# Kernel tuning notes

Measured on AMD Instinct MI355X. Metric: run time of the kernel, lower is better.

Reference implementation:

```python
import jax, jax.numpy as jnp
import numpy as np

B, T, C, H = 4, 2048, 1024, 128  # batch, block_size, n_embds, head_size


def setup_inputs() -> dict:
    key = jax.random.key(0)
    k1, k2, k3, k4 = jax.random.split(key, 4)
    x = jax.random.normal(k1, (B, T, C), dtype=jnp.float32)
    # Linear(n_embds, head_size, bias=False) weights, stored as [C, H] so q = x @ Wq
    s = C ** -0.5
    Wq = jax.random.normal(k2, (C, H), dtype=jnp.float32) * s
    Wk = jax.random.normal(k3, (C, H), dtype=jnp.float32) * s
    Wv = jax.random.normal(k4, (C, H), dtype=jnp.float32) * s
    return {"x": x, "Wq": Wq, "Wk": Wk, "Wv": Wv}


def reference(x, Wq, Wk, Wv):
    # q, k, v projections (no bias)
    q = x @ Wq  # [B, T, H]
    k = x @ Wk  # [B, T, H]
    v = x @ Wv  # [B, T, H]
    scale = q.shape[-1] ** -0.5
    wei = jnp.einsum('btd,bsd->bts', q, k) * scale  # [B, T, T]
    # causal mask: positions where tril == 0 (upper triangle) get -inf
    t = wei.shape[1]
    causal = jnp.tril(jnp.ones((t, t), dtype=bool))
    wei = jnp.where(causal, wei, -jnp.inf)
    # NOTE: source uses F.softmax(wei, dim=1) -> normalize over the QUERY axis
    wei = jax.nn.softmax(wei, axis=1)
    out = wei @ v  # [B, T, H]
    return out
```

## Files before the change

### kernel.cpp

```cpp
#include <hip/hip_runtime.h>
#include <hip/hip_bf16.h>
#include <math.h>

#define B_ 4
#define T_ 2048
#define C_ 1024
#define H_ 128
#define RCHUNK 128
#define NCHUNK (T_ / RCHUNK)
#define NSCH 32

typedef unsigned short u16;
typedef unsigned int   u32;
typedef short short8  __attribute__((ext_vector_type(8)));
typedef short short4v __attribute__((ext_vector_type(4)));
typedef float floatx4 __attribute__((ext_vector_type(4)));

__device__ __forceinline__ u16 f2bf(float f) {
    __hip_bfloat16 h = __float2bfloat16(f);
    union { __hip_bfloat16 h; u16 u; } v; v.h = h; return v.u;
}
__device__ __forceinline__ float bf2f(u16 h) {
    union { u32 u; float f; } v; v.u = ((u32)h) << 16;
    return v.f;
}

__global__ __launch_bounds__(256) void convert_w_kernel(
    const float* __restrict__ Wq, const float* __restrict__ Wk,
    const float* __restrict__ Wv, u16* __restrict__ Wt)
{
    const int k0 = blockIdx.x * 64, n0 = blockIdx.y * 64, widx = blockIdx.z;
    const float* W = (widx == 0) ? Wq : (widx == 1) ? Wk : Wv;

    __shared__ float ts[64][68];
    for (int i = threadIdx.x; i < 64 * 16; i += 256) {
        int r = i >> 4, c4 = i & 15;
        float4 v = *(const float4*)&W[(size_t)(k0 + r) * H_ + n0 + c4 * 4];
        ts[r][c4 * 4 + 0] = v.x; ts[r][c4 * 4 + 1] = v.y;
        ts[r][c4 * 4 + 2] = v.z; ts[r][c4 * 4 + 3] = v.w;
    }
    __syncthreads();
    for (int i = threadIdx.x; i < 64 * 16; i += 256) {
        int n = i >> 4, k4 = i & 15;
        short4v o;
        #pragma unroll
        for (int j = 0; j < 4; ++j) o[j] = (short)f2bf(ts[k4 * 4 + j][n]);
        *(short4v*)&Wt[(size_t)widx * H_ * C_ + (size_t)(n0 + n) * C_ + k0 + k4 * 4] = o;
    }
}

__global__ __launch_bounds__(256) void qkv_gemm_kernel(
    const float* __restrict__ x, const u16* __restrict__ Wt,
    u16* __restrict__ Qb, u16* __restrict__ Kb, u16* __restrict__ Vt)
{
    const int m0   = blockIdx.x * 64;
    const int widx = blockIdx.y;
    const u16* Wg = Wt + (size_t)widx * H_ * C_;

    __shared__ u16 As[64 * 136];
    __shared__ u16 Bs[128 * 136];

    const int w    = threadIdx.x >> 6;
    const int lane = threadIdx.x & 63;
    const int q    = lane >> 4, r = lane & 15;

    floatx4 acc[8] = {};

    for (int k0 = 0; k0 < C_; k0 += 128) {
        for (int i = threadIdx.x; i < 64 * 16; i += 256) {
            int rr = i >> 4, c = i & 15;
            const float* xg = &x[(size_t)(m0 + rr) * C_ + k0 + c * 8];
            float4 a = *(const float4*)xg;
            float4 b = *(const float4*)(xg + 4);
            short8 o;
            o[0]=(short)f2bf(a.x); o[1]=(short)f2bf(a.y);
            o[2]=(short)f2bf(a.z); o[3]=(short)f2bf(a.w);
            o[4]=(short)f2bf(b.x); o[5]=(short)f2bf(b.y);
            o[6]=(short)f2bf(b.z); o[7]=(short)f2bf(b.w);
            *(short8*)&As[rr * 136 + c * 8] = o;
        }
        for (int i = threadIdx.x; i < 128 * 16; i += 256) {
            int rr = i >> 4, c = i & 15;
            *(float4*)&Bs[rr * 136 + c * 8] =
                *(const float4*)&Wg[(size_t)rr * C_ + k0 + c * 8];
        }
        __syncthreads();

        #pragma unroll
        for (int kk = 0; kk < 4; ++kk) {
            short8 af = *(const short8*)&As[(16 * w + r) * 136 + kk * 32 + q * 8];
            #pragma unroll
            for (int nt = 0; nt < 8; ++nt) {
                short8 bf = *(const short8*)&Bs[(16 * nt + r) * 136 + kk * 32 + q * 8];
                acc[nt] = __builtin_amdgcn_mfma_f32_16x16x32_bf16(af, bf, acc[nt], 0, 0, 0);
            }
        }
        __syncthreads();
    }

    if (widx == 2) {
        const int bb  = m0 / T_;
        const int tt0 = (m0 - bb * T_) + 16 * w + q * 4;
        #pragma unroll
        for (int nt = 0; nt < 8; ++nt) {
            short4v o;
            #pragma unroll
            for (int reg = 0; reg < 4; ++reg) o[reg] = (short)f2bf(acc[nt][reg]);
            *(short4v*)&Vt[((size_t)bb * H_ + 16 * nt + r) * T_ + tt0] = o;
        }
    } else {
        u16* dst = (widx == 0) ? Qb : Kb;
        #pragma unroll
        for (int nt = 0; nt < 8; ++nt)
            #pragma unroll
            for (int reg = 0; reg < 4; ++reg) {
                int mm = m0 + 16 * w + q * 4 + reg;
                int nn = 16 * nt + r;
                dst[(size_t)mm * H_ + nn] = f2bf(acc[nt][reg]);
            }
    }
}

__global__ __launch_bounds__(256) void scores_kernel(
    const u16* __restrict__ Qb, const u16* __restrict__ Kb,
    u16* __restrict__ S, float* __restrict__ pm, float* __restrict__ pl)
{
    const int si = blockIdx.x;
    const int ti = blockIdx.y;
    const int b  = blockIdx.z;
    if (si > ti) return;
    const int t0 = ti * 128, s0 = si * 128;
    const bool diag = (si == ti);

    __shared__ u16 smem[2 * 128 * 136];
    u16* Qs = smem;
    u16* Ks = smem + 128 * 136;

    const u16* Qg = Qb + ((size_t)b * T_ + t0) * H_;
    const u16* Kg = Kb + ((size_t)b * T_ + s0) * H_;

    for (int i = threadIdx.x; i < 128 * 16; i += 256) {
        int rr = i >> 4, c = i & 15;
        *(float4*)&Qs[rr * 136 + c * 8] = *(const float4*)&Qg[(size_t)rr * H_ + c * 8];
        *(float4*)&Ks[rr * 136 + c * 8] = *(const float4*)&Kg[(size_t)rr * H_ + c * 8];
    }
    __syncthreads();

    const int w    = threadIdx.x >> 6;
    const int lane = threadIdx.x & 63;
    const int q    = lane >> 4, r = lane & 15;

    floatx4 acc[2][8] = {};
    #pragma unroll
    for (int kk = 0; kk < 4; ++kk) {
        short8 a0 = *(const short8*)&Qs[(32 * w +      r) * 136 + kk * 32 + q * 8];
        short8 a1 = *(const short8*)&Qs[(32 * w + 16 + r) * 136 + kk * 32 + q * 8];
        #pragma unroll
        for (int nt = 0; nt < 8; ++nt) {
            short8 bf = *(const short8*)&Ks[(16 * nt + r) * 136 + kk * 32 + q * 8];
            acc[0][nt] = __builtin_amdgcn_mfma_f32_16x16x32_bf16(a0, bf, acc[0][nt], 0, 0, 0);
            acc[1][nt] = __builtin_amdgcn_mfma_f32_16x16x32_bf16(a1, bf, acc[1][nt], 0, 0, 0);
        }
    }
    __syncthreads();

    u16*   tile = smem;
    float* redm = (float*)(smem + 128 * 136);
    float* redl = redm + 16 * 128;
    float* Mrow = redl + 16 * 128;

    const float scale = 0.08838834764831845f;

    #pragma unroll
    for (int nt = 0; nt < 8; ++nt) {
        const int sl = 16 * nt + r;
        float mx = -INFINITY;
        #pragma unroll
        for (int mt = 0; mt < 2; ++mt)
            #pragma unroll
            for (int reg = 0; reg < 4; ++reg) {
                const int tl = 32 * w + 16 * mt + q * 4 + reg;
                const bool vl = (!diag) || (tl >= sl);
                mx = fmaxf(mx, vl ? acc[mt][nt][reg] : -INFINITY);
            }
        redm[(4 * w + q) * 128 + sl] = mx;
    }
    __syncthreads();

    if (threadIdx.x < 128) {
        const int c = threadIdx.x;
        float M = -INFINITY;
        #pragma unroll
        for (int g = 0; g < 16; ++g) M = fmaxf(M, redm[g * 128 + c]);
        M *= scale;
        Mrow[c] = M;
        pm[((size_t)b * NCHUNK + ti) * T_ + s0 + c] = M;
    }
    __syncthreads();

    #pragma unroll
    for (int nt = 0; nt < 8; ++nt) {
        const int sl = 16 * nt + r;
        const float M = Mrow[sl];
        float sm = 0.f;
        #pragma unroll
        for (int mt = 0; mt < 2; ++mt)
            #pragma unroll
            for (int reg = 0; reg < 4; ++reg) {
                const int tl = 32 * w + 16 * mt + q * 4 + reg;
                const bool vl = (!diag) || (tl >= sl);
                const float e = vl ? __expf(acc[mt][nt][reg] * scale - M) : 0.f;
                sm += e;
                tile[tl * 136 + sl] = f2bf(e);
            }
        redl[(4 * w + q) * 128 + sl] = sm;
    }
    __syncthreads();

    if (threadIdx.x < 128) {
        const int c = threadIdx.x;
        float L = 0.f;
        #pragma unroll
        for (int g = 0; g < 16; ++g) L += redl[g * 128 + c];
        pl[((size_t)b * NCHUNK + ti) * T_ + s0 + c] = L;
    }

    for (int i = threadIdx.x; i < 128 * 16; i += 256) {
        int tl = i >> 4, cc = (i >> 3) & 1, c8 = i & 7;
        u16* Sg = S + (((size_t)b * NSCH + 2 * si + cc) * T_ + t0 + tl) * 64;
        *(float4*)&Sg[c8 * 8] = *(float4*)&tile[tl * 136 + cc * 64 + c8 * 8];
    }
}

__global__ __launch_bounds__(256) void stats_f_kernel(
    const float* __restrict__ pm, const float* __restrict__ pl,
    float* __restrict__ F)
{
    const int idx = blockIdx.x * 256 + threadIdx.x;
    const int b = idx >> 11, s = idx & (T_ - 1);
    const int c0 = s >> 7;
    const float* pmB = pm + (size_t)b * NCHUNK * T_;
    const float* plB = pl + (size_t)b * NCHUNK * T_;

    float M = -INFINITY;
    for (int c = c0; c < NCHUNK; ++c)
        M = fmaxf(M, pmB[(size_t)c * T_ + s]);
    float L = 0.f;
    for (int c = c0; c < NCHUNK; ++c) {
        const float lg = plB[(size_t)c * T_ + s];
        if (lg > 0.f) L += lg * __expf(pmB[(size_t)c * T_ + s] - M);
    }
    const float Li = 1.0f / L;

    float* FB = F + (size_t)b * NCHUNK * T_;
    #pragma unroll
    for (int c = 0; c < NCHUNK; ++c)
        FB[(size_t)c * T_ + s] = (c >= c0) ? __expf(pmB[(size_t)c * T_ + s] - M) * Li : 0.f;
}

#define RST 132
__global__ __launch_bounds__(512) void out_kernel(
    const u16* __restrict__ S, const u16* __restrict__ Vt,
    const float* __restrict__ F, float* __restrict__ out)
{
    const int b   = blockIdx.y;
    const int i   = blockIdx.x;
    const int t0A = i * 16;
    const int t0B = (127 - i) * 16;
    const int ncA = (t0A + 79) >> 6;
    const int ncB = (t0B + 79) >> 6;
    const int nct = ncA + ncB;

    const int w    = threadIdx.x >> 6;
    const int lane = threadIdx.x & 63;
    const int q    = lane >> 4, r = lane & 15;
    const int tA   = t0A + r, tB = t0B + r;

    const u16* SB  = S  + (size_t)b * NSCH * T_ * 64;
    const u16* VtB = Vt + (size_t)b * H_ * T_;

    __shared__ float fsA[T_], fsB[T_];
    __shared__ float red[8][16 * RST];

    floatx4 accA[8] = {}, accB[8] = {};
    short8 sc[2];

    int kcur = w;
    {
        const bool A = kcur < ncA;
        const int ci = A ? kcur : kcur - ncA;
        const u16* Sc = SB + ((size_t)ci * T_ + (A ? tA : tB)) * 64;
        sc[0] = *(const short8*)&Sc[q * 8];
        sc[1] = *(const short8*)&Sc[32 + q * 8];
    }

    const int tiA = t0A >> 7, tiB = t0B >> 7;
    const float* FA = F + ((size_t)b * NCHUNK + tiA) * T_;
    const float* FBg = F + ((size_t)b * NCHUNK + tiB) * T_;
    for (int idx = threadIdx.x * 4; idx < 64 * ncA; idx += 2048)
        *(float4*)&fsA[idx] = *(const float4*)&FA[idx];
    for (int idx = threadIdx.x * 4; idx < 64 * ncB; idx += 2048)
        *(float4*)&fsB[idx] = *(const float4*)&FBg[idx];
    __syncthreads();

    auto body = [&](floatx4 (&acc)[8], const float* fsrow, int s0) {
        #pragma unroll
        for (int kk = 0; kk < 2; ++kk) {
            const int sb = s0 + kk * 32 + q * 8;
            float fv[8];
            *(float4*)&fv[0] = *(const float4*)&fsrow[sb];
            *(float4*)&fv[4] = *(const float4*)&fsrow[sb + 4];
            short8 af;
            #pragma unroll
            for (int j = 0; j < 8; ++j)
                af[j] = (short)f2bf(bf2f((u16)sc[kk][j]) * fv[j]);
            #pragma unroll
            for (int nt = 0; nt < 8; ++nt) {
                short8 bf = *(const short8*)&VtB[(size_t)(16 * nt + r) * T_ + sb];
                acc[nt] = __builtin_amdgcn_mfma_f32_16x16x32_bf16(af, bf, acc[nt], 0, 0, 0);
            }
        }
    };

    while (kcur < nct) {
        const int knx = kcur + 8;
        short8 sn[2];
        if (knx < nct) {
            const bool A = knx < ncA;
            const int ci = A ? knx : knx - ncA;
            const u16* Sc = SB + ((size_t)ci * T_ + (A ? tA : tB)) * 64;
            sn[0] = *(const short8*)&Sc[q * 8];
            sn[1] = *(const short8*)&Sc[32 + q * 8];
        }

        if (kcur < ncA) body(accA, fsA, kcur * 64);
        else            body(accB, fsB, (kcur - ncA) * 64);

        sc[0] = sn[0];
        sc[1] = sn[1];
        kcur = knx;
    }

    #pragma unroll
    for (int nt = 0; nt < 8; ++nt)
        #pragma unroll
        for (int reg = 0; reg < 4; ++reg)
            red[w][(q * 4 + reg) * RST + 16 * nt + r] = accA[nt][reg];
    __syncthreads();

    float* outA = out + ((size_t)b * T_ + t0A) * H_;
    for (int idx = threadIdx.x; idx < 16 * 128; idx += 512) {
        const int row = idx >> 7, col = idx & 127;
        float sum = 0.f;
        #pragma unroll
        for (int g = 0; g < 8; ++g) sum += red[g][row * RST + col];
        outA[idx] = sum;
    }
    __syncthreads();

    #pragma unroll
    for (int nt = 0; nt < 8; ++nt)
        #pragma unroll
        for (int reg = 0; reg < 4; ++reg)
            red[w][(q * 4 + reg) * RST + 16 * nt + r] = accB[nt][reg];
    __syncthreads();

    float* outB = out + ((size_t)b * T_ + t0B) * H_;
    for (int idx = threadIdx.x; idx < 16 * 128; idx += 512) {
        const int row = idx >> 7, col = idx & 127;
        float sum = 0.f;
        #pragma unroll
        for (int g = 0; g < 8; ++g) sum += red[g][row * RST + col];
        outB[idx] = sum;
    }
}

extern "C" void kernel_launch(void* const* d_in, const int* in_sizes, int n_in,
                              void* d_out, int out_size, void* d_ws, size_t ws_size,
                              hipStream_t stream) {
    const float* x  = (const float*)d_in[0];
    const float* Wq = (const float*)d_in[1];
    const float* Wk = (const float*)d_in[2];
    const float* Wv = (const float*)d_in[3];
    float* out = (float*)d_out;

    u16*   Sb   = (u16*)d_ws;
    u16*   Wt   = Sb + (size_t)B_ * T_ * T_;
    u16*   Qb   = Wt + (size_t)3 * H_ * C_;
    u16*   Kb   = Qb + (size_t)B_ * T_ * H_;
    u16*   Vt   = Kb + (size_t)B_ * T_ * H_;
    float* F    = (float*)(Vt + (size_t)B_ * T_ * H_);

    float* pm = (float*)d_out;
    float* pl = pm + (size_t)B_ * NCHUNK * T_;

    convert_w_kernel <<<dim3(C_ / 64, H_ / 64, 3), dim3(256), 0, stream>>>(Wq, Wk, Wv, Wt);
    qkv_gemm_kernel  <<<dim3(B_ * T_ / 64, 3),     dim3(256), 0, stream>>>(x, Wt, Qb, Kb, Vt);
    scores_kernel    <<<dim3(16, 16, B_),          dim3(256), 0, stream>>>(Qb, Kb, Sb, pm, pl);
    stats_f_kernel   <<<dim3(B_ * T_ / 256),       dim3(256), 0, stream>>>(pm, pl, F);
    out_kernel       <<<dim3(64, B_),              dim3(512), 0, stream>>>(Sb, Vt, F, out);
}
```

Before: 161.7 us.

## Fuse scores, stats and output kernels into one cooperative persistent kernel

Merges the scores, stats and output kernels into a single cooperative kernel launched with 256 blocks of 512 threads. Grid-wide syncs separate the three phases, and the scores phase loops over a triangular job list. pm and pl move from the output buffer into workspace. This removes two kernel launches and their gaps, but it adds grid-sync cost, leaves most threads idle in the stats phase (only 32 threads per block), and caps scores-phase parallelism at 256 blocks.

```diff
diff --git a/kernel.cpp b/kernel.cpp
--- a/kernel.cpp
+++ b/kernel.cpp
@@ -1,6 +1,9 @@
 #include <hip/hip_runtime.h>
 #include <hip/hip_bf16.h>
+#include <hip/hip_cooperative_groups.h>
 #include <math.h>
+
+namespace cg = cooperative_groups;
 
 #define B_ 4
 #define T_ 2048
@@ -9,6 +12,8 @@
 #define RCHUNK 128
 #define NCHUNK (T_ / RCHUNK)
 #define NSCH 32
+#define NTILE 136
+#define NJOBS (B_ * NTILE)
 
 typedef unsigned short u16;
 typedef unsigned int   u32;
@@ -121,257 +126,251 @@
     }
 }
 
-__global__ __launch_bounds__(256) void scores_kernel(
+#define RST 132
+__global__ __launch_bounds__(512, 2) void fused_b_kernel(
     const u16* __restrict__ Qb, const u16* __restrict__ Kb,
-    u16* __restrict__ S, float* __restrict__ pm, float* __restrict__ pl)
+    const u16* __restrict__ Vt, u16* __restrict__ S,
+    float* __restrict__ pm, float* __restrict__ pl,
+    float* __restrict__ F, float* __restrict__ out)
 {
-    const int si = blockIdx.x;
-    const int ti = blockIdx.y;
-    const int b  = blockIdx.z;
-    if (si > ti) return;
-    const int t0 = ti * 128, s0 = si * 128;
-    const bool diag = (si == ti);
-
-    __shared__ u16 smem[2 * 128 * 136];
-    u16* Qs = smem;
-    u16* Ks = smem + 128 * 136;
-
-    const u16* Qg = Qb + ((size_t)b * T_ + t0) * H_;
-    const u16* Kg = Kb + ((size_t)b * T_ + s0) * H_;
-
-    for (int i = threadIdx.x; i < 128 * 16; i += 256) {
-        int rr = i >> 4, c = i & 15;
-        *(float4*)&Qs[rr * 136 + c * 8] = *(const float4*)&Qg[(size_t)rr * H_ + c * 8];
-        *(float4*)&Ks[rr * 136 + c * 8] = *(const float4*)&Kg[(size_t)rr * H_ + c * 8];
-    }
-    __syncthreads();
-
-    const int w    = threadIdx.x >> 6;
-    const int lane = threadIdx.x & 63;
+    __shared__ __align__(16) char smem_raw[83968];
+    cg::grid_group grid = cg::this_grid();
+
+    const int blk  = blockIdx.x;
+    const int tid  = threadIdx.x;
+    const int w    = tid >> 6;
+    const int lane = tid & 63;
     const int q    = lane >> 4, r = lane & 15;
-
-    floatx4 acc[2][8] = {};
-    #pragma unroll
-    for (int kk = 0; kk < 4; ++kk) {
-        short8 a0 = *(const short8*)&Qs[(32 * w +      r) * 136 + kk * 32 + q * 8];
-        short8 a1 = *(const short8*)&Qs[(32 * w + 16 + r) * 136 + kk * 32 + q * 8];
-        #pragma unroll
-        for (int nt = 0; nt < 8; ++nt) {
-            short8 bf = *(const short8*)&Ks[(16 * nt + r) * 136 + kk * 32 + q * 8];
-            acc[0][nt] = __builtin_amdgcn_mfma_f32_16x16x32_bf16(a0, bf, acc[0][nt], 0, 0, 0);
-            acc[1][nt] = __builtin_amdgcn_mfma_f32_16x16x32_bf16(a1, bf, acc[1][nt], 0, 0, 0);
-        }
-    }
-    __syncthreads();
-
-    u16*   tile = smem;
-    float* redm = (float*)(smem + 128 * 136);
-    float* redl = redm + 16 * 128;
-    float* Mrow = redl + 16 * 128;
-
     const float scale = 0.08838834764831845f;
 
-    #pragma unroll
-    for (int nt = 0; nt < 8; ++nt) {
-        const int sl = 16 * nt + r;
-        float mx = -INFINITY;
-        #pragma unroll
-        for (int mt = 0; mt < 2; ++mt)
-            #pragma unroll
-            for (int reg = 0; reg < 4; ++reg) {
-                const int tl = 32 * w + 16 * mt + q * 4 + reg;
-                const bool vl = (!diag) || (tl >= sl);
-                mx = fmaxf(mx, vl ? acc[mt][nt][reg] : -INFINITY);
-            }
-        redm[(4 * w + q) * 128 + sl] = mx;
-    }
-    __syncthreads();
-
-    if (threadIdx.x < 128) {
-        const int c = threadIdx.x;
+    {
+        u16* Qs = (u16*)smem_raw;
+        u16* Ks = Qs + 128 * 136;
+
+        for (int job = blk; job < NJOBS; job += 256) {
+            const int b   = job / NTILE;
+            const int rem = job - b * NTILE;
+            int ti = 0;
+            while ((ti + 1) * (ti + 2) / 2 <= rem) ++ti;
+            const int si = rem - ti * (ti + 1) / 2;
+            const int t0 = ti * 128, s0 = si * 128;
+            const bool diag = (si == ti);
+
+            const u16* Qg = Qb + ((size_t)b * T_ + t0) * H_;
+            const u16* Kg = Kb + ((size_t)b * T_ + s0) * H_;
+            for (int i = tid; i < 128 * 16; i += 512) {
+                int rr = i >> 4, c = i & 15;
+                *(float4*)&Qs[rr * 136 + c * 8] = *(const float4*)&Qg[(size_t)rr * H_ + c * 8];
+                *(float4*)&Ks[rr * 136 + c * 8] = *(const float4*)&Kg[(size_t)rr * H_ + c * 8];
+            }
+            __syncthreads();
+
+            floatx4 acc[8] = {};
+            #pragma unroll
+            for (int kk = 0; kk < 4; ++kk) {
+                short8 af = *(const short8*)&Qs[(16 * w + r) * 136 + kk * 32 + q * 8];
+                #pragma unroll
+                for (int nt = 0; nt < 8; ++nt) {
+                    short8 bf = *(const short8*)&Ks[(16 * nt + r) * 136 + kk * 32 + q * 8];
+                    acc[nt] = __builtin_amdgcn_mfma_f32_16x16x32_bf16(af, bf, acc[nt], 0, 0, 0);
+                }
+            }
+            __syncthreads();
+
+            u16*   tile = (u16*)smem_raw;
+            float* redm = (float*)(smem_raw + 34816);
+            float* redl = redm + 32 * 128;
+            float* Mrow = redl + 32 * 128;
+
+            #pragma unroll
+            for (int nt = 0; nt < 8; ++nt) {
+                const int sl = 16 * nt + r;
+                float mx = -INFINITY;
+                #pragma unroll
+                for (int reg = 0; reg < 4; ++reg) {
+                    const int tl = 16 * w + q * 4 + reg;
+                    const bool vl = (!diag) || (tl >= sl);
+                    mx = fmaxf(mx, vl ? acc[nt][reg] : -INFINITY);
+                }
+                redm[(w * 4 + q) * 128 + sl] = mx;
+            }
+            __syncthreads();
+
+            if (tid < 128) {
+                float M = -INFINITY;
+                #pragma unroll
+                for (int g = 0; g < 32; ++g) M = fmaxf(M, redm[g * 128 + tid]);
+                M *= scale;
+                Mrow[tid] = M;
+                pm[((size_t)b * NCHUNK + ti) * T_ + s0 + tid] = M;
+            }
+            __syncthreads();
+
+            #pragma unroll
+            for (int nt = 0; nt < 8; ++nt) {
+                const int sl = 16 * nt + r;
+                const float M = Mrow[sl];
+                float sm = 0.f;
+                #pragma unroll
+                for (int reg = 0; reg < 4; ++reg) {
+                    const int tl = 16 * w + q * 4 + reg;
+                    const bool vl = (!diag) || (tl >= sl);
+                    const float e = vl ? __expf(acc[nt][reg] * scale - M) : 0.f;
+                    sm += e;
+                    tile[tl * 136 + sl] = f2bf(e);
+                }
+                redl[(w * 4 + q) * 128 + sl] = sm;
+            }
+            __syncthreads();
+
+            if (tid < 128) {
+                float L = 0.f;
+                #pragma unroll
+                for (int g = 0; g < 32; ++g) L += redl[g * 128 + tid];
+                pl[((size_t)b * NCHUNK + ti) * T_ + s0 + tid] = L;
+            }
+
+            for (int i = tid; i < 128 * 16; i += 512) {
+                int tl = i >> 4, cc = (i >> 3) & 1, c8 = i & 7;
+                u16* Sg = S + (((size_t)b * NSCH + 2 * si + cc) * T_ + t0 + tl) * 64;
+                *(float4*)&Sg[c8 * 8] = *(float4*)&tile[tl * 136 + cc * 64 + c8 * 8];
+            }
+            __syncthreads();
+        }
+    }
+    grid.sync();
+
+    if (tid < 32) {
+        const int p = blk * 32 + tid;
+        const int b = p >> 11, s = p & (T_ - 1);
+        const int c0 = s >> 7;
+        const float* pmB = pm + (size_t)b * NCHUNK * T_;
+        const float* plB = pl + (size_t)b * NCHUNK * T_;
         float M = -INFINITY;
-        #pragma unroll
-        for (int g = 0; g < 16; ++g) M = fmaxf(M, redm[g * 128 + c]);
-        M *= scale;
-        Mrow[c] = M;
-        pm[((size_t)b * NCHUNK + ti) * T_ + s0 + c] = M;
-    }
-    __syncthreads();
-
-    #pragma unroll
-    for (int nt = 0; nt < 8; ++nt) {
-        const int sl = 16 * nt + r;
-        const float M = Mrow[sl];
-        float sm = 0.f;
-        #pragma unroll
-        for (int mt = 0; mt < 2; ++mt)
-            #pragma unroll
-            for (int reg = 0; reg < 4; ++reg) {
-                const int tl = 32 * w + 16 * mt + q * 4 + reg;
-                const bool vl = (!diag) || (tl >= sl);
-                const float e = vl ? __expf(acc[mt][nt][reg] * scale - M) : 0.f;
-                sm += e;
-                tile[tl * 136 + sl] = f2bf(e);
-            }
-        redl[(4 * w + q) * 128 + sl] = sm;
-    }
-    __syncthreads();
-
-    if (threadIdx.x < 128) {
-        const int c = threadIdx.x;
+        for (int c = c0; c < NCHUNK; ++c)
+            M = fmaxf(M, pmB[(size_t)c * T_ + s]);
         float L = 0.f;
-        #pragma unroll
-        for (int g = 0; g < 16; ++g) L += redl[g * 128 + c];
-        pl[((size_t)b * NCHUNK + ti) * T_ + s0 + c] = L;
-    }
-
-    for (int i = threadIdx.x; i < 128 * 16; i += 256) {
-        int tl = i >> 4, cc = (i >> 3) & 1, c8 = i & 7;
-        u16* Sg = S + (((size_t)b * NSCH + 2 * si + cc) * T_ + t0 + tl) * 64;
-        *(float4*)&Sg[c8 * 8] = *(float4*)&tile[tl * 136 + cc * 64 + c8 * 8];
-    }
-}
-
-__global__ __launch_bounds__(256) void stats_f_kernel(
-    const float* __restrict__ pm, const float* __restrict__ pl,
-    float* __restrict__ F)
-{
-    const int idx = blockIdx.x * 256 + threadIdx.x;
-    const int b = idx >> 11, s = idx & (T_ - 1);
-    const int c0 = s >> 7;
-    const float* pmB = pm + (size_t)b * NCHUNK * T_;
-    const float* plB = pl + (size_t)b * NCHUNK * T_;
-
-    float M = -INFINITY;
-    for (int c = c0; c < NCHUNK; ++c)
-        M = fmaxf(M, pmB[(size_t)c * T_ + s]);
-    float L = 0.f;
-    for (int c = c0; c < NCHUNK; ++c) {
-        const float lg = plB[(size_t)c * T_ + s];
-        if (lg > 0.f) L += lg * __expf(pmB[(size_t)c * T_ + s] - M);
-    }
-    const float Li = 1.0f / L;
-
-    float* FB = F + (size_t)b * NCHUNK * T_;
-    #pragma unroll
-    for (int c = 0; c < NCHUNK; ++c)
-        FB[(size_t)c * T_ + s] = (c >= c0) ? __expf(pmB[(size_t)c * T_ + s] - M) * Li : 0.f;
-}
-
-#define RST 132
-__global__ __launch_bounds__(512) void out_kernel(
-    const u16* __restrict__ S, const u16* __restrict__ Vt,
-    const float* __restrict__ F, float* __restrict__ out)
-{
-    const int b   = blockIdx.y;
-    const int i   = blockIdx.x;
-    const int t0A = i * 16;
-    const int t0B = (127 - i) * 16;
-    const int ncA = (t0A + 79) >> 6;
-    const int ncB = (t0B + 79) >> 6;
-    const int nct = ncA + ncB;
-
-    const int w    = threadIdx.x >> 6;
-    const int lane = threadIdx.x & 63;
-    const int q    = lane >> 4, r = lane & 15;
-    const int tA   = t0A + r, tB = t0B + r;
-
-    const u16* SB  = S  + (size_t)b * NSCH * T_ * 64;
-    const u16* VtB = Vt + (size_t)b * H_ * T_;
-
-    __shared__ float fsA[T_], fsB[T_];
-    __shared__ float red[8][16 * RST];
-
-    floatx4 accA[8] = {}, accB[8] = {};
-    short8 sc[2];
-
-    int kcur = w;
+        for (int c = c0; c < NCHUNK; ++c) {
+            const float lg = plB[(size_t)c * T_ + s];
+            if (lg > 0.f) L += lg * __expf(pmB[(size_t)c * T_ + s] - M);
+        }
+        const float Li = 1.0f / L;
+        float* FB = F + (size_t)b * NCHUNK * T_;
+        #pragma unroll
+        for (int c = 0; c < NCHUNK; ++c)
+            FB[(size_t)c * T_ + s] = (c >= c0) ? __expf(pmB[(size_t)c * T_ + s] - M) * Li : 0.f;
+    }
+    grid.sync();
+
     {
-        const bool A = kcur < ncA;
-        const int ci = A ? kcur : kcur - ncA;
-        const u16* Sc = SB + ((size_t)ci * T_ + (A ? tA : tB)) * 64;
-        sc[0] = *(const short8*)&Sc[q * 8];
-        sc[1] = *(const short8*)&Sc[32 + q * 8];
-    }
-
-    const int tiA = t0A >> 7, tiB = t0B >> 7;
-    const float* FA = F + ((size_t)b * NCHUNK + tiA) * T_;
-    const float* FBg = F + ((size_t)b * NCHUNK + tiB) * T_;
-    for (int idx = threadIdx.x * 4; idx < 64 * ncA; idx += 2048)
-        *(float4*)&fsA[idx] = *(const float4*)&FA[idx];
-    for (int idx = threadIdx.x * 4; idx < 64 * ncB; idx += 2048)
-        *(float4*)&fsB[idx] = *(const float4*)&FBg[idx];
-    __syncthreads();
-
-    auto body = [&](floatx4 (&acc)[8], const float* fsrow, int s0) {
-        #pragma unroll
-        for (int kk = 0; kk < 2; ++kk) {
-            const int sb = s0 + kk * 32 + q * 8;
-            float fv[8];
-            *(float4*)&fv[0] = *(const float4*)&fsrow[sb];
-            *(float4*)&fv[4] = *(const float4*)&fsrow[sb + 4];
-            short8 af;
-            #pragma unroll
-            for (int j = 0; j < 8; ++j)
-                af[j] = (short)f2bf(bf2f((u16)sc[kk][j]) * fv[j]);
-            #pragma unroll
-            for (int nt = 0; nt < 8; ++nt) {
-                short8 bf = *(const short8*)&VtB[(size_t)(16 * nt + r) * T_ + sb];
-                acc[nt] = __builtin_amdgcn_mfma_f32_16x16x32_bf16(af, bf, acc[nt], 0, 0, 0);
-            }
-        }
-    };
-
-    while (kcur < nct) {
-        const int knx = kcur + 8;
-        short8 sn[2];
-        if (knx < nct) {
-            const bool A = knx < ncA;
-            const int ci = A ? knx : knx - ncA;
+        const int b   = blk >> 6;
+        const int i   = blk & 63;
+        const int t0A = i * 16;
+        const int t0B = (127 - i) * 16;
+        const int ncA = (t0A + 79) >> 6;
+        const int ncB = (t0B + 79) >> 6;
+        const int nct = ncA + ncB;
+
+        const int tA = t0A + r, tB = t0B + r;
+
+        const u16* SB  = S  + (size_t)b * NSCH * T_ * 64;
+        const u16* VtB = Vt + (size_t)b * H_ * T_;
+
+        float* fsA = (float*)smem_raw;
+        float* fsB = fsA + T_;
+        float* red = fsB + T_;
+
+        floatx4 accA[8] = {}, accB[8] = {};
+        short8 sc[2];
+
+        int kcur = w;
+        {
+            const bool A = kcur < ncA;
+            const int ci = A ? kcur : kcur - ncA;
             const u16* Sc = SB + ((size_t)ci * T_ + (A ? tA : tB)) * 64;
-            sn[0] = *(const short8*)&Sc[q * 8];
-            sn[1] = *(const short8*)&Sc[32 + q * 8];
-        }
-
-        if (kcur < ncA) body(accA, fsA, kcur * 64);
-        else            body(accB, fsB, (kcur - ncA) * 64);
-
-        sc[0] = sn[0];
-        sc[1] = sn[1];
-        kcur = knx;
-    }
-
-    #pragma unroll
-    for (int nt = 0; nt < 8; ++nt)
-        #pragma unroll
-        for (int reg = 0; reg < 4; ++reg)
-            red[w][(q * 4 + reg) * RST + 16 * nt + r] = accA[nt][reg];
-    __syncthreads();
-
-    float* outA = out + ((size_t)b * T_ + t0A) * H_;
-    for (int idx = threadIdx.x; idx < 16 * 128; idx += 512) {
-        const int row = idx >> 7, col = idx & 127;
-        float sum = 0.f;
-        #pragma unroll
-        for (int g = 0; g < 8; ++g) sum += red[g][row * RST + col];
-        outA[idx] = sum;
-    }
-    __syncthreads();
-
-    #pragma unroll
-    for (int nt = 0; nt < 8; ++nt)
-        #pragma unroll
-        for (int reg = 0; reg < 4; ++reg)
-            red[w][(q * 4 + reg) * RST + 16 * nt + r] = accB[nt][reg];
-    __syncthreads();
-
-    float* outB = out + ((size_t)b * T_ + t0B) * H_;
-    for (int idx = threadIdx.x; idx < 16 * 128; idx += 512) {
-        const int row = idx >> 7, col = idx & 127;
-        float sum = 0.f;
-        #pragma unroll
-        for (int g = 0; g < 8; ++g) sum += red[g][row * RST + col];
-        outB[idx] = sum;
+            sc[0] = *(const short8*)&Sc[q * 8];
+            sc[1] = *(const short8*)&Sc[32 + q * 8];
+        }
+
+        const int tiA = t0A >> 7, tiB = t0B >> 7;
+        const float* FA  = F + ((size_t)b * NCHUNK + tiA) * T_;
+        const float* FBg = F + ((size_t)b * NCHUNK + tiB) * T_;
+        for (int idx = tid * 4; idx < 64 * ncA; idx += 2048)
+            *(float4*)&fsA[idx] = *(const float4*)&FA[idx];
+        for (int idx = tid * 4; idx < 64 * ncB; idx += 2048)
+            *(float4*)&fsB[idx] = *(const float4*)&FBg[idx];
+        __syncthreads();
+
+        auto body = [&](floatx4 (&acc)[8], const float* fsrow, int s0) {
+            #pragma unroll
+            for (int kk = 0; kk < 2; ++kk) {
+                const int sb = s0 + kk * 32 + q * 8;
+                float fv[8];
+                *(float4*)&fv[0] = *(const float4*)&fsrow[sb];
+                *(float4*)&fv[4] = *(const float4*)&fsrow[sb + 4];
+                short8 af;
+                #pragma unroll
+                for (int j = 0; j < 8; ++j)
+                    af[j] = (short)f2bf(bf2f((u16)sc[kk][j]) * fv[j]);
+                #pragma unroll
+                for (int nt = 0; nt < 8; ++nt) {
+                    short8 bf = *(const short8*)&VtB[(size_t)(16 * nt + r) * T_ + sb];
+                    acc[nt] = __builtin_amdgcn_mfma_f32_16x16x32_bf16(af, bf, acc[nt], 0, 0, 0);
+                }
+            }
+        };
+
+        while (kcur < nct) {
+            const int knx = kcur + 8;
+            short8 sn[2];
+            if (knx < nct) {
+                const bool A = knx < ncA;
+                const int ci = A ? knx : knx - ncA;
+                const u16* Sc = SB + ((size_t)ci * T_ + (A ? tA : tB)) * 64;
+                sn[0] = *(const short8*)&Sc[q * 8];
+                sn[1] = *(const short8*)&Sc[32 + q * 8];
+            }
+
+            if (kcur < ncA) body(accA, fsA, kcur * 64);
+            else            body(accB, fsB, (kcur - ncA) * 64);
+
+            sc[0] = sn[0];
+            sc[1] = sn[1];
+            kcur = knx;
+        }
+
+        #pragma unroll
+        for (int nt = 0; nt < 8; ++nt)
+            #pragma unroll
+            for (int reg = 0; reg < 4; ++reg)
+                red[w * 16 * RST + (q * 4 + reg) * RST + 16 * nt + r] = accA[nt][reg];
+        __syncthreads();
+
+        float* outA = out + ((size_t)b * T_ + t0A) * H_;
+        for (int idx = tid; idx < 16 * 128; idx += 512) {
+            const int row = idx >> 7, col = idx & 127;
+            float sum = 0.f;
+            #pragma unroll
+            for (int g = 0; g < 8; ++g) sum += red[g * 16 * RST + row * RST + col];
+            outA[idx] = sum;
+        }
+        __syncthreads();
+
+        #pragma unroll
+        for (int nt = 0; nt < 8; ++nt)
+            #pragma unroll
+            for (int reg = 0; reg < 4; ++reg)
+                red[w * 16 * RST + (q * 4 + reg) * RST + 16 * nt + r] = accB[nt][reg];
+        __syncthreads();
+
+        float* outB = out + ((size_t)b * T_ + t0B) * H_;
+        for (int idx = tid; idx < 16 * 128; idx += 512) {
+            const int row = idx >> 7, col = idx & 127;
+            float sum = 0.f;
+            #pragma unroll
+            for (int g = 0; g < 8; ++g) sum += red[g * 16 * RST + row * RST + col];
+            outB[idx] = sum;
+        }
     }
 }
 
@@ -389,14 +388,15 @@
     u16*   Qb   = Wt + (size_t)3 * H_ * C_;
     u16*   Kb   = Qb + (size_t)B_ * T_ * H_;
     u16*   Vt   = Kb + (size_t)B_ * T_ * H_;
-    float* F    = (float*)(Vt + (size_t)B_ * T_ * H_);
-
-    float* pm = (float*)d_out;
-    float* pl = pm + (size_t)B_ * NCHUNK * T_;
+    float* pm   = (float*)(Vt + (size_t)B_ * T_ * H_);
+    float* pl   = pm + (size_t)B_ * NCHUNK * T_;
+    float* F    = pl + (size_t)B_ * NCHUNK * T_;
 
     convert_w_kernel <<<dim3(C_ / 64, H_ / 64, 3), dim3(256), 0, stream>>>(Wq, Wk, Wv, Wt);
     qkv_gemm_kernel  <<<dim3(B_ * T_ / 64, 3),     dim3(256), 0, stream>>>(x, Wt, Qb, Kb, Vt);
-    scores_kernel    <<<dim3(16, 16, B_),          dim3(256), 0, stream>>>(Qb, Kb, Sb, pm, pl);
-    stats_f_kernel   <<<dim3(B_ * T_ / 256),       dim3(256), 0, stream>>>(pm, pl, F);
-    out_kernel       <<<dim3(64, B_),              dim3(512), 0, stream>>>(Sb, Vt, F, out);
-}
+
+    void* args[] = { (void*)&Qb, (void*)&Kb, (void*)&Vt, (void*)&Sb,
+                     (void*)&pm, (void*)&pl, (void*)&F, (void*)&out };
+    hipLaunchCooperativeKernel((const void*)fused_b_kernel,
+                               dim3(256), dim3(512), args, 0, stream);
+}
```

Measured after the change: 233.4 us. 1.44x slower.
